# Kernel optimization log

Hardware: AMD Instinct MI355X
Metric: run time of the kernel (lower is better)

The kernel has to match this reference:

```python
import jax, jax.numpy as jnp
import numpy as np

D_MODEL = 1024
NUM_HEADS = 16
THETA = 10000.0
BATCH = 2
SEQ = 2048


def _rope(x, pos, theta):
    # x: (b, h, l, d), pos: (l,)
    d = x.shape[-1]
    half = d // 2
    inv_freq = theta ** (-(jnp.arange(half, dtype=x.dtype) / half))  # theta^(-2k/d)
    ang = pos.astype(x.dtype)[:, None] * inv_freq[None, :]  # (l, half)
    cos, sin = jnp.cos(ang), jnp.sin(ang)
    x1, x2 = x[..., ::2], x[..., 1::2]
    r1 = x1 * cos - x2 * sin
    r2 = x1 * sin + x2 * cos
    return jnp.stack([r1, r2], axis=-1).reshape(x.shape)


def setup_inputs() -> dict:
    key = jax.random.key(0)
    k1, k2, k3 = jax.random.split(key, 3)
    x = jax.random.normal(k1, (BATCH, SEQ, D_MODEL), dtype=jnp.float32)
    W_kqv = jax.random.normal(k2, (3 * D_MODEL, D_MODEL), dtype=jnp.float32) * (1.0 / np.sqrt(D_MODEL))
    W_o = jax.random.normal(k3, (D_MODEL, D_MODEL), dtype=jnp.float32) * (1.0 / np.sqrt(D_MODEL))
    return {"x": x, "W_kqv": W_kqv, "W_o": W_o}


def reference(x, W_kqv, W_o):
    b, L, _ = x.shape
    h = NUM_HEADS
    d = D_MODEL // h
    kqv = x @ W_kqv.T  # (b, l, 3*d_model)
    K, Q, V = jnp.split(kqv, 3, axis=-1)  # chunk order in source: K, Q, V
    # (b, l, h*d) -> (b, h, l, d)
    Q = Q.reshape(b, L, h, d).transpose(0, 2, 1, 3)
    K = K.reshape(b, L, h, d).transpose(0, 2, 1, 3)
    V = V.reshape(b, L, h, d).transpose(0, 2, 1, 3)
    pos = jnp.arange(L)
    Q = _rope(Q, pos, THETA)
    K = _rope(K, pos, THETA)
    scores = jnp.einsum('bhqd,bhkd->bhqk', Q, K) / jnp.sqrt(jnp.asarray(d, x.dtype))
    causal = jnp.tril(jnp.ones((L, L), dtype=bool))
    scores = jnp.where(causal, scores, jnp.finfo(scores.dtype).min)
    probs = jax.nn.softmax(scores, axis=-1)
    out = jnp.einsum('bhqk,bhkd->bhqd', probs, V)
    out = out.transpose(0, 2, 1, 3).reshape(b, L, h * d)
    return out @ W_o.T
```

## Files before the change

### kernel.cpp

```cpp
#include <hip/hip_runtime.h>
#include <hip/hip_bf16.h>
#include <stdint.h>

#define BATCH 2
#define SEQ 2048
#define DMODEL 1024
#define NHEADS 16
#define HDIM 64
#define MROWS (BATCH*SEQ)
#define N3 (3*DMODEL)

typedef __attribute__((ext_vector_type(8))) __bf16 bf16x8;
typedef __attribute__((ext_vector_type(4))) float f32x4;

__device__ __forceinline__ ushort f2b(float f) {
  uint32_t u = __builtin_bit_cast(uint32_t, f);
  uint32_t r = (u + 0x7FFFu + ((u >> 16) & 1u)) >> 16;
  return (ushort)r;
}
__device__ __forceinline__ float b2f(ushort h) {
  return __builtin_bit_cast(float, (uint32_t)h << 16);
}
__device__ __forceinline__ float exp2_hw(float x) {
  float r;
  asm("v_exp_f32 %0, %1" : "=v"(r) : "v"(x));
  return r;
}
__device__ __forceinline__ uint32_t cvtpk(float a, float b) {
  uint32_t r;
  asm("v_cvt_pk_bf16_f32 %0, %1, %2" : "=v"(r) : "v"(a), "v"(b));
  return r;
}

__global__ void f2b3_kernel(const float* __restrict__ a, const float* __restrict__ b,
                            const float* __restrict__ c,
                            ushort* __restrict__ oa, ushort* __restrict__ ob,
                            ushort* __restrict__ oc, int na, int nb, int nc) {
  int i = blockIdx.x * blockDim.x + threadIdx.x;
  const float* src; ushort* dst; int off;
  if (i < na)           { src = a; dst = oa; off = i; }
  else if (i < na + nb) { src = b; dst = ob; off = i - na; }
  else if (i < na + nb + nc) { src = c; dst = oc; off = i - na - nb; }
  else return;
  float4 v = ((const float4*)src)[off];
  uint32_t lo = cvtpk(v.x, v.y), hi_ = cvtpk(v.z, v.w);
  ((uint2*)dst)[off] = make_uint2(lo, hi_);
}

template<int OUTF>
__global__ __launch_bounds__(256)
void gemm_bt(const ushort* __restrict__ A, const ushort* __restrict__ Bw,
             void* __restrict__ Cv, int M, int N, int K) {
  __shared__ __align__(16) ushort As[128*32];
  __shared__ __align__(16) ushort Bs[128*32];
  const int tid  = threadIdx.x;
  const int wid  = tid >> 6;
  const int lane = tid & 63;
  const int wr   = wid >> 1, wc = wid & 1;
  const int l16  = lane & 15, lhi = lane >> 4;
  const int nb   = N >> 7;
  const int brow = (blockIdx.x / nb) << 7;
  const int bcol = (blockIdx.x % nb) << 7;

  f32x4 acc[4][4] = {};

  for (int k0 = 0; k0 < K; k0 += 32) {
    __syncthreads();
#pragma unroll
    for (int it = 0; it < 2; ++it) {
      const int cb    = (wid * 2 + it) * 64;
      const int chunk = cb + lane;
      const int r     = chunk >> 2;
      const int c8    = chunk & 3;
      const ushort* ga = A  + (size_t)(brow + r) * K + k0 + c8 * 8;
      const ushort* gb = Bw + (size_t)(bcol + r) * K + k0 + c8 * 8;
      __builtin_amdgcn_global_load_lds(
          (const __attribute__((address_space(1))) void*)ga,
          (__attribute__((address_space(3))) void*)(As + cb * 8), 16, 0, 0);
      __builtin_amdgcn_global_load_lds(
          (const __attribute__((address_space(1))) void*)gb,
          (__attribute__((address_space(3))) void*)(Bs + cb * 8), 16, 0, 0);
    }
    __syncthreads();

    bf16x8 af[4], bfr[4];
#pragma unroll
    for (int m = 0; m < 4; ++m)
      af[m] = *(const bf16x8*)(As + (wr*64 + m*16 + l16)*32 + lhi*8);
#pragma unroll
    for (int n = 0; n < 4; ++n)
      bfr[n] = *(const bf16x8*)(Bs + (wc*64 + n*16 + l16)*32 + lhi*8);
#pragma unroll
    for (int m = 0; m < 4; ++m)
#pragma unroll
      for (int n = 0; n < 4; ++n)
        acc[m][n] = __builtin_amdgcn_mfma_f32_16x16x32_bf16(af[m], bfr[n], acc[m][n], 0, 0, 0);
  }

#pragma unroll
  for (int m = 0; m < 4; ++m)
#pragma unroll
    for (int n = 0; n < 4; ++n)
#pragma unroll
      for (int r = 0; r < 4; ++r) {
        const int row = brow + wr*64 + m*16 + lhi*4 + r;
        const int col = bcol + wc*64 + n*16 + l16;
        if (OUTF) ((float*)Cv)[(size_t)row * N + col] = acc[m][n][r];
        else      ((ushort*)Cv)[(size_t)row * N + col] = f2b(acc[m][n][r]);
      }
}

__global__ __launch_bounds__(256)
void prep_kernel(const ushort* __restrict__ kqv,
                 ushort* __restrict__ qb, ushort* __restrict__ kb, ushort* __restrict__ vt) {
  __shared__ ushort tile[64][65];
  if (blockIdx.x < 1024) {
    int bid = blockIdx.x;
    int lt = bid & 31, bh = bid >> 5;
    int b = bh >> 4, h = bh & 15;
    int tid = threadIdx.x;
    int r = tid >> 2, cq = tid & 3;
    size_t gbase = ((size_t)(b * SEQ + lt * 64 + r)) * N3 + 2 * DMODEL + h * HDIM + cq * 16;
#pragma unroll
    for (int j = 0; j < 16; ++j) tile[r][cq * 16 + j] = kqv[gbase + j];
    __syncthreads();
    int d = tid >> 2;
    size_t obase = ((size_t)(bh * HDIM + d)) * SEQ + lt * 64 + cq * 16;
#pragma unroll
    for (int j = 0; j < 16; ++j) vt[obase + j] = tile[cq * 16 + j][d];
  } else {
    const float SC = 0.18033688011112042f;
    int idx = (blockIdx.x - 1024) * 256 + threadIdx.x;
    int i  = idx & 31;
    int h  = (idx >> 5) & 15;
    int bl = idx >> 9;
    int l  = bl & (SEQ - 1);
    int b  = bl >> 11;
    float inv = exp2f((float)i * -0.4152410118609203f);
    float ang = (float)l * inv;
    float s, c;
    sincosf(ang, &s, &c);
    size_t base = (size_t)bl * N3 + h * HDIM + 2 * i;
    uint32_t kp = *(const uint32_t*)(kqv + base);
    uint32_t qp = *(const uint32_t*)(kqv + base + DMODEL);
    float k1 = b2f((ushort)(kp & 0xffff)), k2 = b2f((ushort)(kp >> 16));
    float q1 = b2f((ushort)(qp & 0xffff)), q2 = b2f((ushort)(qp >> 16));
    float kr1 = k1 * c - k2 * s, kr2 = k1 * s + k2 * c;
    float qr1 = (q1 * c - q2 * s) * SC, qr2 = (q1 * s + q2 * c) * SC;
    size_t ob = ((size_t)(b * NHEADS + h) * SEQ + l) * HDIM + 2 * i;
    *(uint32_t*)(kb + ob) = cvtpk(kr1, kr2);
    *(uint32_t*)(qb + ob) = cvtpk(qr1, qr2);
  }
}

__global__ __launch_bounds__(256, 2)
void attn_kernel(const ushort* __restrict__ qb, const ushort* __restrict__ kb,
                 const ushort* __restrict__ vt, ushort* __restrict__ ao) {
  __shared__ __align__(16) ushort Kbuf[2][4096];
  __shared__ __align__(16) ushort Vbuf[2][4096];
  __shared__ __align__(16) ushort plds[4][1024];
  const int bid = blockIdx.x;
  const int bh = bid & 31;
  const int p  = bid >> 5;
  const int qtA = p, qtB = 31 - p;

  const int wid = threadIdx.x >> 6, lane = threadIdx.x & 63;
  const int l16 = lane & 15, lhi = lane >> 4;
  const int r0A = qtA * 64 + wid * 16;
  const int r0B = qtB * 64 + wid * 16;

  const ushort* Q  = qb + (size_t)bh * SEQ * HDIM;
  const ushort* Kp = kb + (size_t)bh * SEQ * HDIM;
  const ushort* Vp = vt + (size_t)bh * HDIM * SEQ;

  bf16x8 qfA[2], qfB[2];
#pragma unroll
  for (int kc = 0; kc < 2; ++kc) {
    qfA[kc] = *(const bf16x8*)(Q + (size_t)(r0A + l16) * HDIM + kc * 32 + lhi * 8);
    qfB[kc] = *(const bf16x8*)(Q + (size_t)(r0B + l16) * HDIM + kc * 32 + lhi * 8);
  }

  float mqA = -3.0e38f, lsA = 0.0f, mqB = -3.0e38f, lsB = 0.0f;
  f32x4 oA[4] = {}, oB[4] = {};

  char* pbase = (char*)&plds[wid][0];
  const int swz = (l16 & 7) << 4;

  auto STAGE = [&](int buf, int kt) {
    ushort* kd = &Kbuf[buf][0];
    ushort* vd = &Vbuf[buf][0];
    const ushort* kg = Kp + (size_t)kt * 64 * HDIM;
    const ushort* vg = Vp + kt * 64;
#pragma unroll
    for (int it = 0; it < 2; ++it) {
      const int cb = it * 256 + wid * 64;
      const int ci = cb + lane;
      const int row = ci >> 3;
      const int sl  = (ci & 7) ^ (row & 7);
      __builtin_amdgcn_global_load_lds(
          (const __attribute__((address_space(1))) void*)(kg + row * HDIM + sl * 8),
          (__attribute__((address_space(3))) void*)(kd + cb * 8), 16, 0, 0);
      __builtin_amdgcn_global_load_lds(
          (const __attribute__((address_space(1))) void*)(vg + (size_t)row * SEQ + sl * 8),
          (__attribute__((address_space(3))) void*)(vd + cb * 8), 16, 0, 0);
    }
  };

  auto BODY = [&](const char* kc_, const char* vc_, bf16x8 (&qf)[2],
                  float& mq, float& lsq, f32x4 (&o)[4], int r0, int qt, int kt) {
    f32x4 s[4];
#pragma unroll
    for (int n = 0; n < 4; ++n) {
      const int kvr = n * 16 + l16;
      bf16x8 kf0 = *(const bf16x8*)(kc_ + kvr*128 + ((lhi     ^ (kvr&7)) * 16));
      bf16x8 kf1 = *(const bf16x8*)(kc_ + kvr*128 + (((4+lhi) ^ (kvr&7)) * 16));
      f32x4 z = 0.0f;
      z = __builtin_amdgcn_mfma_f32_16x16x32_bf16(kf0, qf[0], z, 0, 0, 0);
      z = __builtin_amdgcn_mfma_f32_16x16x32_bf16(kf1, qf[1], z, 0, 0, 0);
      s[n] = z;
    }
    if (kt == qt) {
#pragma unroll
      for (int n = 0; n < 4; ++n)
#pragma unroll
        for (int r = 0; r < 4; ++r)
          if (kt*64 + n*16 + lhi*4 + r > r0 + l16) s[n][r] = -3.0e38f;
    }
    float t0 = fmaxf(fmaxf(s[0][0], s[0][1]), fmaxf(s[0][2], s[0][3]));
    float t1 = fmaxf(fmaxf(s[1][0], s[1][1]), fmaxf(s[1][2], s[1][3]));
    float t2 = fmaxf(fmaxf(s[2][0], s[2][1]), fmaxf(s[2][2], s[2][3]));
    float t3 = fmaxf(fmaxf(s[3][0], s[3][1]), fmaxf(s[3][2], s[3][3]));
    float pmx = fmaxf(fmaxf(t0, t1), fmaxf(t2, t3));
    pmx = fmaxf(pmx, __shfl_xor(pmx, 16));
    pmx = fmaxf(pmx, __shfl_xor(pmx, 32));

    if (!__all(pmx <= mq)) {
      float mn = fmaxf(mq, pmx);
      float alpha = exp2_hw(mq - mn);
      mq = mn;
      lsq *= alpha;
      float alphaT[4];
#pragma unroll
      for (int r = 0; r < 4; ++r)
        alphaT[r] = __shfl(alpha, lhi * 4 + r);
#pragma unroll
      for (int f = 0; f < 4; ++f)
#pragma unroll
        for (int r = 0; r < 4; ++r)
          o[f][r] *= alphaT[r];
    }

    float ps = 0.0f;
#pragma unroll
    for (int n = 0; n < 4; ++n)
#pragma unroll
      for (int r = 0; r < 4; ++r) {
        float pv = exp2_hw(s[n][r] - mq);
        s[n][r] = pv;
        ps += pv;
      }
    ps += __shfl_xor(ps, 16);
    ps += __shfl_xor(ps, 32);
    lsq += ps;

#pragma unroll
    for (int n = 0; n < 4; ++n) {
      uint32_t w0 = cvtpk(s[n][0], s[n][1]);
      uint32_t w1 = cvtpk(s[n][2], s[n][3]);
      int kvloc = n*16 + lhi*4;
      *(uint32_t*)(pbase + ((l16*128 + kvloc*2) ^ swz))       = w0;
      *(uint32_t*)(pbase + ((l16*128 + (kvloc+2)*2) ^ swz))   = w1;
    }
    bf16x8 pa0 = *(const bf16x8*)(pbase + ((l16*128 + 0*64 + lhi*16) ^ swz));
    bf16x8 pa1 = *(const bf16x8*)(pbase + ((l16*128 + 1*64 + lhi*16) ^ swz));

#pragma unroll
    for (int f = 0; f < 4; ++f) {
      const int dr = f * 16 + l16;
      bf16x8 vf0 = *(const bf16x8*)(vc_ + dr*128 + ((lhi     ^ (dr&7)) * 16));
      bf16x8 vf1 = *(const bf16x8*)(vc_ + dr*128 + (((4+lhi) ^ (dr&7)) * 16));
      o[f] = __builtin_amdgcn_mfma_f32_16x16x32_bf16(pa0, vf0, o[f], 0, 0, 0);
      o[f] = __builtin_amdgcn_mfma_f32_16x16x32_bf16(pa1, vf1, o[f], 0, 0, 0);
    }
  };

  int cur = 0;
  STAGE(0, 0);
  __syncthreads();

  for (int kt = 0; kt <= qtB; ++kt) {
    if (kt < qtB) STAGE(cur ^ 1, kt + 1);
    const char* kc_ = (const char*)&Kbuf[cur][0];
    const char* vc_ = (const char*)&Vbuf[cur][0];
    BODY(kc_, vc_, qfB, mqB, lsB, oB, r0B, qtB, kt);
    if (kt <= qtA)
      BODY(kc_, vc_, qfA, mqA, lsA, oA, r0A, qtA, kt);
    __syncthreads();
    cur ^= 1;
  }

  const int b = bh >> 4, h = bh & 15;
  float invA = 1.0f / lsA, invB = 1.0f / lsB;
#pragma unroll
  for (int r = 0; r < 4; ++r) {
    float wA = __shfl(invA, lhi * 4 + r);
    float wB = __shfl(invB, lhi * 4 + r);
    size_t baseA = ((size_t)(b * SEQ + r0A + lhi*4 + r)) * DMODEL + h * HDIM + l16;
    size_t baseB = ((size_t)(b * SEQ + r0B + lhi*4 + r)) * DMODEL + h * HDIM + l16;
#pragma unroll
    for (int f = 0; f < 4; ++f) {
      ao[baseA + f*16] = f2b(oA[f][r] * wA);
      ao[baseB + f*16] = f2b(oB[f][r] * wB);
    }
  }
}

extern "C" void kernel_launch(void* const* d_in, const int* in_sizes, int n_in,
                              void* d_out, int out_size, void* d_ws, size_t ws_size,
                              hipStream_t stream) {
  const float* x    = (const float*)d_in[0];
  const float* wkqv = (const float*)d_in[1];
  const float* wo   = (const float*)d_in[2];
  float* out = (float*)d_out;

  ushort* xb   = (ushort*)d_ws;
  ushort* wkb  = xb  + (size_t)MROWS * DMODEL;
  ushort* wob  = wkb + (size_t)N3 * DMODEL;
  ushort* kqv  = wob + (size_t)DMODEL * DMODEL;
  ushort* qb   = kqv + (size_t)MROWS * N3;
  ushort* kb   = qb  + (size_t)MROWS * DMODEL;
  ushort* vt   = kb  + (size_t)MROWS * DMODEL;
  ushort* attn = xb;

  int nx = MROWS * DMODEL / 4, nw = N3 * DMODEL / 4, no = DMODEL * DMODEL / 4;
  f2b3_kernel<<<(nx + nw + no) / 256, 256, 0, stream>>>(x, wkqv, wo, xb, wkb, wob, nx, nw, no);

  gemm_bt<0><<<(MROWS/128) * (N3/128), 256, 0, stream>>>(xb, wkb, (void*)kqv, MROWS, N3, DMODEL);

  prep_kernel<<<1024 + (MROWS * NHEADS * 32) / 256, 256, 0, stream>>>(kqv, qb, kb, vt);

  attn_kernel<<<512, 256, 0, stream>>>(qb, kb, vt, attn);

  gemm_bt<1><<<(MROWS/128) * (DMODEL/128), 256, 0, stream>>>(attn, wob, (void*)out, MROWS, DMODEL, DMODEL);
}
```

Before: 126.6 us.

## Pair adjacent query tiles per block and interleave their QK/PV MFMAs

Changes the work assignment so each block handles two adjacent query tiles (2i, 2i+1) instead of a balanced pair (p, 31-p). Blocks with the largest tiles are scheduled first. The two tiles share every K/V tile load, and their MFMAs are interleaved in one fused loop with separate P scratch buffers. Occupancy in the launch bounds is raised from 2 to 3. This aims to cut repeated K fragment reads and improve instruction-level parallelism, but it gives up the per-block causal load balance and depends on LPT-style scheduling and the higher occupancy to keep CUs busy.

```diff
diff --git a/kernel.cpp b/kernel.cpp
--- a/kernel.cpp
+++ b/kernel.cpp
@@ -153,16 +153,16 @@
   }
 }
 
-__global__ __launch_bounds__(256, 2)
+__global__ __launch_bounds__(256, 3)
 void attn_kernel(const ushort* __restrict__ qb, const ushort* __restrict__ kb,
                  const ushort* __restrict__ vt, ushort* __restrict__ ao) {
   __shared__ __align__(16) ushort Kbuf[2][4096];
   __shared__ __align__(16) ushort Vbuf[2][4096];
-  __shared__ __align__(16) ushort plds[4][1024];
-  const int bid = blockIdx.x;
-  const int bh = bid & 31;
-  const int p  = bid >> 5;
-  const int qtA = p, qtB = 31 - p;
+  __shared__ __align__(16) ushort plds[4][2048];
+  const int g  = blockIdx.x;
+  const int bh = g & 31;
+  const int i  = 15 - (g >> 5);
+  const int qtA = 2 * i, qtB = 2 * i + 1;
 
   const int wid = threadIdx.x >> 6, lane = threadIdx.x & 63;
   const int l16 = lane & 15, lhi = lane >> 4;
@@ -183,7 +183,8 @@
   float mqA = -3.0e38f, lsA = 0.0f, mqB = -3.0e38f, lsB = 0.0f;
   f32x4 oA[4] = {}, oB[4] = {};
 
-  char* pbase = (char*)&plds[wid][0];
+  char* pB = (char*)&plds[wid][0];
+  char* pA = (char*)&plds[wid][1024];
   const int swz = (l16 & 7) << 4;
 
   auto STAGE = [&](int buf, int kt) {
@@ -206,19 +207,8 @@
     }
   };
 
-  auto BODY = [&](const char* kc_, const char* vc_, bf16x8 (&qf)[2],
-                  float& mq, float& lsq, f32x4 (&o)[4], int r0, int qt, int kt) {
-    f32x4 s[4];
-#pragma unroll
-    for (int n = 0; n < 4; ++n) {
-      const int kvr = n * 16 + l16;
-      bf16x8 kf0 = *(const bf16x8*)(kc_ + kvr*128 + ((lhi     ^ (kvr&7)) * 16));
-      bf16x8 kf1 = *(const bf16x8*)(kc_ + kvr*128 + (((4+lhi) ^ (kvr&7)) * 16));
-      f32x4 z = 0.0f;
-      z = __builtin_amdgcn_mfma_f32_16x16x32_bf16(kf0, qf[0], z, 0, 0, 0);
-      z = __builtin_amdgcn_mfma_f32_16x16x32_bf16(kf1, qf[1], z, 0, 0, 0);
-      s[n] = z;
-    }
+  auto SOFT = [&](f32x4 (&s)[4], float& mq, float& lsq, f32x4 (&o)[4],
+                  int r0, int qt, int kt, char* pb) {
     if (kt == qt) {
 #pragma unroll
       for (int n = 0; n < 4; ++n)
@@ -268,35 +258,85 @@
       uint32_t w0 = cvtpk(s[n][0], s[n][1]);
       uint32_t w1 = cvtpk(s[n][2], s[n][3]);
       int kvloc = n*16 + lhi*4;
-      *(uint32_t*)(pbase + ((l16*128 + kvloc*2) ^ swz))       = w0;
-      *(uint32_t*)(pbase + ((l16*128 + (kvloc+2)*2) ^ swz))   = w1;
-    }
-    bf16x8 pa0 = *(const bf16x8*)(pbase + ((l16*128 + 0*64 + lhi*16) ^ swz));
-    bf16x8 pa1 = *(const bf16x8*)(pbase + ((l16*128 + 1*64 + lhi*16) ^ swz));
+      *(uint32_t*)(pb + ((l16*128 + kvloc*2) ^ swz))       = w0;
+      *(uint32_t*)(pb + ((l16*128 + (kvloc+2)*2) ^ swz))   = w1;
+    }
+  };
+
+  int cur = 0;
+  STAGE(0, 0);
+  __syncthreads();
+
+  for (int kt = 0; kt <= qtA; ++kt) {
+    STAGE(cur ^ 1, kt + 1);
+
+    const char* kc_ = (const char*)&Kbuf[cur][0];
+    const char* vc_ = (const char*)&Vbuf[cur][0];
+
+    f32x4 sB[4], sA[4];
+#pragma unroll
+    for (int n = 0; n < 4; ++n) {
+      const int kvr = n * 16 + l16;
+      bf16x8 kf0 = *(const bf16x8*)(kc_ + kvr*128 + ((lhi     ^ (kvr&7)) * 16));
+      bf16x8 kf1 = *(const bf16x8*)(kc_ + kvr*128 + (((4+lhi) ^ (kvr&7)) * 16));
+      f32x4 zB = 0.0f, zA = 0.0f;
+      zB = __builtin_amdgcn_mfma_f32_16x16x32_bf16(kf0, qfB[0], zB, 0, 0, 0);
+      zB = __builtin_amdgcn_mfma_f32_16x16x32_bf16(kf1, qfB[1], zB, 0, 0, 0);
+      zA = __builtin_amdgcn_mfma_f32_16x16x32_bf16(kf0, qfA[0], zA, 0, 0, 0);
+      zA = __builtin_amdgcn_mfma_f32_16x16x32_bf16(kf1, qfA[1], zA, 0, 0, 0);
+      sB[n] = zB; sA[n] = zA;
+    }
+
+    SOFT(sB, mqB, lsB, oB, r0B, qtB, kt, pB);
+    SOFT(sA, mqA, lsA, oA, r0A, qtA, kt, pA);
+
+    bf16x8 paB0 = *(const bf16x8*)(pB + ((l16*128 + 0*64 + lhi*16) ^ swz));
+    bf16x8 paB1 = *(const bf16x8*)(pB + ((l16*128 + 1*64 + lhi*16) ^ swz));
+    bf16x8 paA0 = *(const bf16x8*)(pA + ((l16*128 + 0*64 + lhi*16) ^ swz));
+    bf16x8 paA1 = *(const bf16x8*)(pA + ((l16*128 + 1*64 + lhi*16) ^ swz));
 
 #pragma unroll
     for (int f = 0; f < 4; ++f) {
       const int dr = f * 16 + l16;
       bf16x8 vf0 = *(const bf16x8*)(vc_ + dr*128 + ((lhi     ^ (dr&7)) * 16));
       bf16x8 vf1 = *(const bf16x8*)(vc_ + dr*128 + (((4+lhi) ^ (dr&7)) * 16));
-      o[f] = __builtin_amdgcn_mfma_f32_16x16x32_bf16(pa0, vf0, o[f], 0, 0, 0);
-      o[f] = __builtin_amdgcn_mfma_f32_16x16x32_bf16(pa1, vf1, o[f], 0, 0, 0);
-    }
-  };
-
-  int cur = 0;
-  STAGE(0, 0);
-  __syncthreads();
-
-  for (int kt = 0; kt <= qtB; ++kt) {
-    if (kt < qtB) STAGE(cur ^ 1, kt + 1);
+      oB[f] = __builtin_amdgcn_mfma_f32_16x16x32_bf16(paB0, vf0, oB[f], 0, 0, 0);
+      oB[f] = __builtin_amdgcn_mfma_f32_16x16x32_bf16(paB1, vf1, oB[f], 0, 0, 0);
+      oA[f] = __builtin_amdgcn_mfma_f32_16x16x32_bf16(paA0, vf0, oA[f], 0, 0, 0);
+      oA[f] = __builtin_amdgcn_mfma_f32_16x16x32_bf16(paA1, vf1, oA[f], 0, 0, 0);
+    }
+
+    __syncthreads();
+    cur ^= 1;
+  }
+
+  {
+    const int kt = qtB;
     const char* kc_ = (const char*)&Kbuf[cur][0];
     const char* vc_ = (const char*)&Vbuf[cur][0];
-    BODY(kc_, vc_, qfB, mqB, lsB, oB, r0B, qtB, kt);
-    if (kt <= qtA)
-      BODY(kc_, vc_, qfA, mqA, lsA, oA, r0A, qtA, kt);
-    __syncthreads();
-    cur ^= 1;
+
+    f32x4 sB[4];
+#pragma unroll
+    for (int n = 0; n < 4; ++n) {
+      const int kvr = n * 16 + l16;
+      bf16x8 kf0 = *(const bf16x8*)(kc_ + kvr*128 + ((lhi     ^ (kvr&7)) * 16));
+      bf16x8 kf1 = *(const bf16x8*)(kc_ + kvr*128 + (((4+lhi) ^ (kvr&7)) * 16));
+      f32x4 z = 0.0f;
+      z = __builtin_amdgcn_mfma_f32_16x16x32_bf16(kf0, qfB[0], z, 0, 0, 0);
+      z = __builtin_amdgcn_mfma_f32_16x16x32_bf16(kf1, qfB[1], z, 0, 0, 0);
+      sB[n] = z;
+    }
+    SOFT(sB, mqB, lsB, oB, r0B, qtB, kt, pB);
+    bf16x8 paB0 = *(const bf16x8*)(pB + ((l16*128 + 0*64 + lhi*16) ^ swz));
+    bf16x8 paB1 = *(const bf16x8*)(pB + ((l16*128 + 1*64 + lhi*16) ^ swz));
+#pragma unroll
+    for (int f = 0; f < 4; ++f) {
+      const int dr = f * 16 + l16;
+      bf16x8 vf0 = *(const bf16x8*)(vc_ + dr*128 + ((lhi     ^ (dr&7)) * 16));
+      bf16x8 vf1 = *(const bf16x8*)(vc_ + dr*128 + (((4+lhi) ^ (dr&7)) * 16));
+      oB[f] = __builtin_amdgcn_mfma_f32_16x16x32_bf16(paB0, vf0, oB[f], 0, 0, 0);
+      oB[f] = __builtin_amdgcn_mfma_f32_16x16x32_bf16(paB1, vf1, oB[f], 0, 0, 0);
+    }
   }
 
   const int b = bh >> 4, h = bh & 15;
```

Result: slower. 139.7 us (+10.3%).

## Split paired query tiles across wave pairs with 32-row subtiles per wave

Applied to the files above, without the earlier changes.

In the attention kernel, each wave used to process 16 rows of both paired query tiles (early and late). Now waves 0–1 take the early tile and waves 2–3 the late tile, with each wave handling two 16-row subtiles that share the same K fragments. The occupancy hint rises from 2 to 3 blocks per CU, and the P scratch in shared memory doubles. The aim is more MFMA work per K/V fragment load and more blocks resident at once. The cost is an uneven split inside each block: waves on the early tile sit idle at barriers while the late-tile waves keep iterating, which lengthens the block's critical path.

```diff
diff --git a/kernel.cpp b/kernel.cpp
--- a/kernel.cpp
+++ b/kernel.cpp
@@ -153,37 +153,38 @@
   }
 }
 
-__global__ __launch_bounds__(256, 2)
+__global__ __launch_bounds__(256, 3)
 void attn_kernel(const ushort* __restrict__ qb, const ushort* __restrict__ kb,
                  const ushort* __restrict__ vt, ushort* __restrict__ ao) {
   __shared__ __align__(16) ushort Kbuf[2][4096];
   __shared__ __align__(16) ushort Vbuf[2][4096];
-  __shared__ __align__(16) ushort plds[4][1024];
-  const int bid = blockIdx.x;
-  const int bh = bid & 31;
-  const int p  = bid >> 5;
+  __shared__ __align__(16) ushort plds[4][2048];
+  const int g  = blockIdx.x;
+  const int bh = g & 31;
+  const int p  = g >> 5;
   const int qtA = p, qtB = 31 - p;
 
   const int wid = threadIdx.x >> 6, lane = threadIdx.x & 63;
   const int l16 = lane & 15, lhi = lane >> 4;
-  const int r0A = qtA * 64 + wid * 16;
-  const int r0B = qtB * 64 + wid * 16;
+  const int qt = (wid >> 1) ? qtB : qtA;
+  const int r0 = qt * 64 + (wid & 1) * 32;
 
   const ushort* Q  = qb + (size_t)bh * SEQ * HDIM;
   const ushort* Kp = kb + (size_t)bh * SEQ * HDIM;
   const ushort* Vp = vt + (size_t)bh * HDIM * SEQ;
 
-  bf16x8 qfA[2], qfB[2];
-#pragma unroll
-  for (int kc = 0; kc < 2; ++kc) {
-    qfA[kc] = *(const bf16x8*)(Q + (size_t)(r0A + l16) * HDIM + kc * 32 + lhi * 8);
-    qfB[kc] = *(const bf16x8*)(Q + (size_t)(r0B + l16) * HDIM + kc * 32 + lhi * 8);
-  }
-
-  float mqA = -3.0e38f, lsA = 0.0f, mqB = -3.0e38f, lsB = 0.0f;
-  f32x4 oA[4] = {}, oB[4] = {};
-
-  char* pbase = (char*)&plds[wid][0];
+  bf16x8 qf[2][2];
+#pragma unroll
+  for (int s = 0; s < 2; ++s)
+#pragma unroll
+    for (int kc = 0; kc < 2; ++kc)
+      qf[s][kc] = *(const bf16x8*)(Q + (size_t)(r0 + s*16 + l16) * HDIM + kc * 32 + lhi * 8);
+
+  float mq0 = -3.0e38f, ls0 = 0.0f, mq1 = -3.0e38f, ls1 = 0.0f;
+  f32x4 o0[4] = {}, o1[4] = {};
+
+  char* pb0 = (char*)&plds[wid][0];
+  char* pb1 = (char*)&plds[wid][1024];
   const int swz = (l16 & 7) << 4;
 
   auto STAGE = [&](int buf, int kt) {
@@ -206,25 +207,14 @@
     }
   };
 
-  auto BODY = [&](const char* kc_, const char* vc_, bf16x8 (&qf)[2],
-                  float& mq, float& lsq, f32x4 (&o)[4], int r0, int qt, int kt) {
-    f32x4 s[4];
-#pragma unroll
-    for (int n = 0; n < 4; ++n) {
-      const int kvr = n * 16 + l16;
-      bf16x8 kf0 = *(const bf16x8*)(kc_ + kvr*128 + ((lhi     ^ (kvr&7)) * 16));
-      bf16x8 kf1 = *(const bf16x8*)(kc_ + kvr*128 + (((4+lhi) ^ (kvr&7)) * 16));
-      f32x4 z = 0.0f;
-      z = __builtin_amdgcn_mfma_f32_16x16x32_bf16(kf0, qf[0], z, 0, 0, 0);
-      z = __builtin_amdgcn_mfma_f32_16x16x32_bf16(kf1, qf[1], z, 0, 0, 0);
-      s[n] = z;
-    }
+  auto SOFT = [&](f32x4 (&s)[4], float& mq, float& lsq, f32x4 (&o)[4],
+                  int r0s, int kt, char* pb) {
     if (kt == qt) {
 #pragma unroll
       for (int n = 0; n < 4; ++n)
 #pragma unroll
         for (int r = 0; r < 4; ++r)
-          if (kt*64 + n*16 + lhi*4 + r > r0 + l16) s[n][r] = -3.0e38f;
+          if (kt*64 + n*16 + lhi*4 + r > r0s + l16) s[n][r] = -3.0e38f;
     }
     float t0 = fmaxf(fmaxf(s[0][0], s[0][1]), fmaxf(s[0][2], s[0][3]));
     float t1 = fmaxf(fmaxf(s[1][0], s[1][1]), fmaxf(s[1][2], s[1][3]));
@@ -268,19 +258,8 @@
       uint32_t w0 = cvtpk(s[n][0], s[n][1]);
       uint32_t w1 = cvtpk(s[n][2], s[n][3]);
       int kvloc = n*16 + lhi*4;
-      *(uint32_t*)(pbase + ((l16*128 + kvloc*2) ^ swz))       = w0;
-      *(uint32_t*)(pbase + ((l16*128 + (kvloc+2)*2) ^ swz))   = w1;
-    }
-    bf16x8 pa0 = *(const bf16x8*)(pbase + ((l16*128 + 0*64 + lhi*16) ^ swz));
-    bf16x8 pa1 = *(const bf16x8*)(pbase + ((l16*128 + 1*64 + lhi*16) ^ swz));
-
-#pragma unroll
-    for (int f = 0; f < 4; ++f) {
-      const int dr = f * 16 + l16;
-      bf16x8 vf0 = *(const bf16x8*)(vc_ + dr*128 + ((lhi     ^ (dr&7)) * 16));
-      bf16x8 vf1 = *(const bf16x8*)(vc_ + dr*128 + (((4+lhi) ^ (dr&7)) * 16));
-      o[f] = __builtin_amdgcn_mfma_f32_16x16x32_bf16(pa0, vf0, o[f], 0, 0, 0);
-      o[f] = __builtin_amdgcn_mfma_f32_16x16x32_bf16(pa1, vf1, o[f], 0, 0, 0);
+      *(uint32_t*)(pb + ((l16*128 + kvloc*2) ^ swz))       = w0;
+      *(uint32_t*)(pb + ((l16*128 + (kvloc+2)*2) ^ swz))   = w1;
     }
   };
 
@@ -290,27 +269,61 @@
 
   for (int kt = 0; kt <= qtB; ++kt) {
     if (kt < qtB) STAGE(cur ^ 1, kt + 1);
-    const char* kc_ = (const char*)&Kbuf[cur][0];
-    const char* vc_ = (const char*)&Vbuf[cur][0];
-    BODY(kc_, vc_, qfB, mqB, lsB, oB, r0B, qtB, kt);
-    if (kt <= qtA)
-      BODY(kc_, vc_, qfA, mqA, lsA, oA, r0A, qtA, kt);
+
+    if (kt <= qt) {
+      const char* kc_ = (const char*)&Kbuf[cur][0];
+      const char* vc_ = (const char*)&Vbuf[cur][0];
+
+      f32x4 s0[4], s1[4];
+#pragma unroll
+      for (int n = 0; n < 4; ++n) {
+        const int kvr = n * 16 + l16;
+        bf16x8 kf0 = *(const bf16x8*)(kc_ + kvr*128 + ((lhi     ^ (kvr&7)) * 16));
+        bf16x8 kf1 = *(const bf16x8*)(kc_ + kvr*128 + (((4+lhi) ^ (kvr&7)) * 16));
+        f32x4 z0 = 0.0f, z1 = 0.0f;
+        z0 = __builtin_amdgcn_mfma_f32_16x16x32_bf16(kf0, qf[0][0], z0, 0, 0, 0);
+        z0 = __builtin_amdgcn_mfma_f32_16x16x32_bf16(kf1, qf[0][1], z0, 0, 0, 0);
+        z1 = __builtin_amdgcn_mfma_f32_16x16x32_bf16(kf0, qf[1][0], z1, 0, 0, 0);
+        z1 = __builtin_amdgcn_mfma_f32_16x16x32_bf16(kf1, qf[1][1], z1, 0, 0, 0);
+        s0[n] = z0; s1[n] = z1;
+      }
+
+      SOFT(s0, mq0, ls0, o0, r0,      kt, pb0);
+      SOFT(s1, mq1, ls1, o1, r0 + 16, kt, pb1);
+
+      bf16x8 pa00 = *(const bf16x8*)(pb0 + ((l16*128 + 0*64 + lhi*16) ^ swz));
+      bf16x8 pa01 = *(const bf16x8*)(pb0 + ((l16*128 + 1*64 + lhi*16) ^ swz));
+      bf16x8 pa10 = *(const bf16x8*)(pb1 + ((l16*128 + 0*64 + lhi*16) ^ swz));
+      bf16x8 pa11 = *(const bf16x8*)(pb1 + ((l16*128 + 1*64 + lhi*16) ^ swz));
+
+#pragma unroll
+      for (int f = 0; f < 4; ++f) {
+        const int dr = f * 16 + l16;
+        bf16x8 vf0 = *(const bf16x8*)(vc_ + dr*128 + ((lhi     ^ (dr&7)) * 16));
+        bf16x8 vf1 = *(const bf16x8*)(vc_ + dr*128 + (((4+lhi) ^ (dr&7)) * 16));
+        o0[f] = __builtin_amdgcn_mfma_f32_16x16x32_bf16(pa00, vf0, o0[f], 0, 0, 0);
+        o0[f] = __builtin_amdgcn_mfma_f32_16x16x32_bf16(pa01, vf1, o0[f], 0, 0, 0);
+        o1[f] = __builtin_amdgcn_mfma_f32_16x16x32_bf16(pa10, vf0, o1[f], 0, 0, 0);
+        o1[f] = __builtin_amdgcn_mfma_f32_16x16x32_bf16(pa11, vf1, o1[f], 0, 0, 0);
+      }
+    }
+
     __syncthreads();
     cur ^= 1;
   }
 
   const int b = bh >> 4, h = bh & 15;
-  float invA = 1.0f / lsA, invB = 1.0f / lsB;
+  float inv0 = 1.0f / ls0, inv1 = 1.0f / ls1;
 #pragma unroll
   for (int r = 0; r < 4; ++r) {
-    float wA = __shfl(invA, lhi * 4 + r);
-    float wB = __shfl(invB, lhi * 4 + r);
-    size_t baseA = ((size_t)(b * SEQ + r0A + lhi*4 + r)) * DMODEL + h * HDIM + l16;
-    size_t baseB = ((size_t)(b * SEQ + r0B + lhi*4 + r)) * DMODEL + h * HDIM + l16;
+    float w0 = __shfl(inv0, lhi * 4 + r);
+    float w1 = __shfl(inv1, lhi * 4 + r);
+    size_t base0 = ((size_t)(b * SEQ + r0 + lhi*4 + r)) * DMODEL + h * HDIM + l16;
+    size_t base1 = ((size_t)(b * SEQ + r0 + 16 + lhi*4 + r)) * DMODEL + h * HDIM + l16;
 #pragma unroll
     for (int f = 0; f < 4; ++f) {
-      ao[baseA + f*16] = f2b(oA[f][r] * wA);
-      ao[baseB + f*16] = f2b(oB[f][r] * wB);
+      ao[base0 + f*16] = f2b(o0[f][r] * w0);
+      ao[base1 + f*16] = f2b(o1[f][r] * w1);
     }
   }
 }
```

After: 140.8 us. +11.2%, slower.
